# Performance work log

Hardware: AMD Instinct MI355X
Metric: run time of the kernel (lower is better)

Reference implementation:

```python
import jax, jax.numpy as jnp
import numpy as np

EMBED_DIM = 1024
NUM_HEADS = 16
HEAD_DIM = EMBED_DIM // NUM_HEADS
ROPE_BASE = 10000.0


def rotate_half(x):
    # interleaved variant: pairs (x0,x1) -> (-x1, x0)
    x1 = x[..., ::2]
    x2 = x[..., 1::2]
    return jnp.stack((-x2, x1), axis=-1).reshape(x.shape)


def rope_tables(T, dim, dtype):
    inv_freq = 1.0 / (ROPE_BASE ** (jnp.arange(0, dim, 2, dtype=jnp.float32) / dim))
    t = jnp.arange(T, dtype=jnp.float32)
    freqs = t[:, None] * inv_freq[None, :]          # [T, dim/2]
    emb = jnp.concatenate((freqs, freqs), axis=-1)  # [T, dim]
    return jnp.cos(emb).astype(dtype), jnp.sin(emb).astype(dtype)


def setup_inputs() -> dict:
    key = jax.random.key(0)
    kx, kq, ko = jax.random.split(key, 3)
    B, T, D = 2, 2048, EMBED_DIM
    x = jax.random.normal(kx, (B, T, D), dtype=jnp.float32)
    s = 1.0 / np.sqrt(D)
    Wqkv = jax.random.normal(kq, (D, 3 * D), dtype=jnp.float32) * s
    Wout = jax.random.normal(ko, (D, D), dtype=jnp.float32) * s
    return {"x": x, "Wqkv": Wqkv, "Wout": Wout}


def reference(x, Wqkv, Wout):
    B, T, D = x.shape
    H, hd = NUM_HEADS, HEAD_DIM
    qkv = x @ Wqkv                                   # [B,T,3D]
    q, k, v = jnp.split(qkv, 3, axis=-1)
    q = q.reshape(B, T, H, hd).transpose(0, 2, 1, 3)  # [B,H,T,hd]
    k = k.reshape(B, T, H, hd).transpose(0, 2, 1, 3)
    v = v.reshape(B, T, H, hd).transpose(0, 2, 1, 3)
    cos, sin = rope_tables(T, hd, x.dtype)           # [T,hd]
    cos = cos[None, None, :, :]
    sin = sin[None, None, :, :]
    q = q * cos + rotate_half(q) * sin
    k = k * cos + rotate_half(k) * sin
    scale = 1.0 / np.sqrt(hd).astype(np.float32)
    attn = jnp.einsum('bhtd,bhsd->bhts', q, k) * scale  # [B,H,T,T]
    attn = jax.nn.softmax(attn, axis=-1)
    out = jnp.einsum('bhts,bhsd->bhtd', attn, v)     # [B,H,T,hd]
    out = out.transpose(0, 2, 1, 3).reshape(B, T, D)
    return out @ Wout
```

## Files before the change

kernel.cpp:

```cpp
#include <hip/hip_runtime.h>
#include <hip/hip_bf16.h>
#include <stdint.h>


typedef unsigned short u16;
typedef short bf16x8 __attribute__((ext_vector_type(8)));
typedef float f32x4  __attribute__((ext_vector_type(4)));
typedef float f32x16 __attribute__((ext_vector_type(16)));

#if defined(__has_builtin) && __has_builtin(__builtin_amdgcn_exp2f)
#define EXP2F(x) __builtin_amdgcn_exp2f(x)
#else
#define EXP2F(x) exp2f(x)
#endif

__device__ __forceinline__ u16 f2b(float f) {
  uint32_t u = __float_as_uint(f);
  u += 0x7fffu + ((u >> 16) & 1u);
  return (u16)(u >> 16);
}
__device__ __forceinline__ uint32_t pkbf(float a, float b) {
  __hip_bfloat162 h = __float22bfloat162_rn(make_float2(a, b));
  union { __hip_bfloat162 h2; uint32_t u; } cv; cv.h2 = h;
  return cv.u;
}

__device__ __forceinline__ void gl2lds16(const void* g, void* l) {
  __builtin_amdgcn_global_load_lds(
      (const __attribute__((address_space(1))) unsigned int*)g,
      (__attribute__((address_space(3))) unsigned int*)l, 16, 0, 0);
}

__global__ void sniff_kernel(const u16* x, int* flag) {
  __shared__ int cnt;
  if (threadIdx.x == 0) cnt = 0;
  __syncthreads();
  int c = 0;
  for (int i = threadIdx.x; i < 4096; i += 256) {
    float a = fabsf(__uint_as_float(((uint32_t)x[2*i]) << 16));
    if (a > 1e-3f && a < 100.f) c++;
  }
  atomicAdd(&cnt, c);
  __syncthreads();
  if (threadIdx.x == 0) *flag = (cnt > 2048) ? 1 : 0;
}

__device__ __forceinline__ void tr_tile(const void* src, u16* dst, int Kd, int N,
                                        int n0, int k0, int isb, u16* Lt, int tid)
{
  const int r = tid >> 2, cseg = (tid & 3) << 4;
  u16 t[16];
  if (isb) {
    const u16* s = (const u16*)src + (size_t)(k0 + r) * N + n0 + cseg;
    *(uint4*)&t[0] = *(const uint4*)s;
    *(uint4*)&t[8] = *(const uint4*)(s + 8);
  } else {
    const float* s = (const float*)src + (size_t)(k0 + r) * N + n0 + cseg;
    #pragma unroll
    for (int j = 0; j < 4; j++) {
      float4 v = *(const float4*)(s + j * 4);
      t[j*4+0] = f2b(v.x); t[j*4+1] = f2b(v.y); t[j*4+2] = f2b(v.z); t[j*4+3] = f2b(v.w);
    }
  }
  #pragma unroll
  for (int j = 0; j < 16; j++) Lt[(cseg + j) * 72 + r] = t[j];
  __syncthreads();
  const int n = tid >> 2, kseg = (tid & 3) << 4;
  uint4 u0 = *(const uint4*)&Lt[n * 72 + kseg];
  uint4 u1 = *(const uint4*)&Lt[n * 72 + kseg + 8];
  u16* d = dst + (size_t)(n0 + n) * Kd + k0 + kseg;
  *(uint4*)d = u0;
  *(uint4*)(d + 8) = u1;
}

__global__ __launch_bounds__(256) void prep_kernel(
    const void* __restrict__ x, const void* __restrict__ wqkv,
    const void* __restrict__ wout, const int* __restrict__ flag,
    u16* __restrict__ Xb, u16* __restrict__ Wqkvt, u16* __restrict__ Woutt,
    float2* __restrict__ CS)
{
  __shared__ u16 Lt[64 * 72];
  const int isb = *flag;
  const int bid = blockIdx.x, tid = threadIdx.x;
  if (bid < 2048) {
    const size_t i = ((size_t)bid * 256 + tid) * 8;
    if (isb) {
      *(uint4*)&Xb[i] = *(const uint4*)((const u16*)x + i);
    } else {
      const float* s = (const float*)x + i;
      float4 a = *(const float4*)s, b = *(const float4*)(s + 4);
      uint4 p;
      p.x = pkbf(a.x, a.y); p.y = pkbf(a.z, a.w);
      p.z = pkbf(b.x, b.y); p.w = pkbf(b.z, b.w);
      *(uint4*)&Xb[i] = p;
    }
  } else if (bid < 2816) {
    const int b = bid - 2048;
    tr_tile(wqkv, Wqkvt, 1024, 3072, (b % 48) * 64, (b / 48) * 64, isb, Lt, tid);
  } else if (bid < 3072) {
    const int b = bid - 2816;
    tr_tile(wout, Woutt, 1024, 1024, (b % 16) * 64, (b / 16) * 64, isb, Lt, tid);
  } else {
    const int idx = (bid - 3072) * 256 + tid;
    const int t = idx >> 5, f = idx & 31;
    float invf = __expf(-(float)f * 0.2878231366242557f);
    float th = (float)t * invf;
    float sn, cs;
    sincosf(th, &sn, &cs);
    CS[idx] = make_float2(cs, sn);
  }
}

__global__ __launch_bounds__(256) void qkv_kernel(
    const u16* __restrict__ Xb, const u16* __restrict__ Wt,
    const float2* __restrict__ CS,
    u16* __restrict__ Q, u16* __restrict__ K, u16* __restrict__ Vt)
{
  __shared__ u16 As[128 * 64];
  __shared__ u16 Bs[128 * 64];
  const int tid = threadIdx.x;
  const int n0 = blockIdx.x * 128;
  const int m0 = blockIdx.y * 128;
  const int w = tid >> 6, l = tid & 63, lr = l & 15, lq = l >> 4;
  const int mrow0 = (w & 1) * 64;
  const int ncol0 = (w >> 1) * 64;
  const int srow = tid >> 3;
  const int gseg = (tid & 7) ^ (srow & 7);

  const int col0 = n0 + ncol0;
  const int sec = col0 >> 10;
  const int isv = (sec == 2);
  const int h = (col0 >> 6) & 15;

  f32x4 acc[4][4] = {};

  for (int k0 = 0; k0 < 1024; k0 += 64) {
    __syncthreads();
    #pragma unroll
    for (int rd = 0; rd < 4; rd++) {
      const int row = srow + rd * 32;
      gl2lds16(Xb + (size_t)(m0 + row) * 1024 + k0 + gseg * 8, &As[tid * 8 + rd * 2048]);
      gl2lds16(Wt + (size_t)(n0 + row) * 1024 + k0 + gseg * 8, &Bs[tid * 8 + rd * 2048]);
    }
    __syncthreads();
    #pragma unroll
    for (int kc = 0; kc < 2; kc++) {
      bf16x8 af[4], bf[4];
      #pragma unroll
      for (int i = 0; i < 4; i++) {
        const int seg = ((kc << 2) | lq) ^ (lr & 7);
        af[i] = *(const bf16x8*)&As[(mrow0 + i * 16 + lr) * 64 + seg * 8];
        bf[i] = *(const bf16x8*)&Bs[(ncol0 + i * 16 + lr) * 64 + seg * 8];
      }
      if (isv) {
        #pragma unroll
        for (int mb = 0; mb < 4; mb++)
          #pragma unroll
          for (int nb = 0; nb < 4; nb++)
            acc[mb][nb] = __builtin_amdgcn_mfma_f32_16x16x32_bf16(af[mb], bf[nb], acc[mb][nb], 0, 0, 0);
      } else {
        #pragma unroll
        for (int mb = 0; mb < 4; mb++)
          #pragma unroll
          for (int nb = 0; nb < 4; nb++)
            acc[mb][nb] = __builtin_amdgcn_mfma_f32_16x16x32_bf16(bf[nb], af[mb], acc[mb][nb], 0, 0, 0);
      }
    }
  }

  if (isv) {
    #pragma unroll
    for (int mb = 0; mb < 4; mb++) {
      const int row0 = m0 + mrow0 + mb * 16 + lq * 4;
      const int b = row0 >> 11, t0 = row0 & 2047;
      const int tp = (t0 & ~12) | ((t0 & 4) << 1) | ((t0 & 8) >> 1);
      #pragma unroll
      for (int nb = 0; nb < 4; nb++) {
        const int d = nb * 16 + lr;
        uint2 uv;
        uv.x = pkbf(acc[mb][nb][0], acc[mb][nb][1]);
        uv.y = pkbf(acc[mb][nb][2], acc[mb][nb][3]);
        *(uint2*)&Vt[(((size_t)b * 16 + h) * 64 + d) * 2048 + tp] = uv;
      }
    }
  } else {
    u16* dst = (sec == 0) ? Q : K;
    const float qscale = 0.125f * 1.44269504f;
    #pragma unroll
    for (int mb = 0; mb < 4; mb++) {
      const int m = m0 + mrow0 + mb * 16 + lr;
      const int b = m >> 11, t = m & 2047;
      const float* csrow = (const float*)(CS + t * 32);
      #pragma unroll
      for (int nb = 0; nb < 4; nb++) {
        const int d = nb * 16 + lq * 4;
        const int fb = d & 31;
        f32x4 c01 = *(const f32x4*)(csrow + 2 * fb);
        f32x4 c23 = *(const f32x4*)(csrow + 2 * fb + 4);
        float v0 = acc[mb][nb][0], v1 = acc[mb][nb][1];
        float v2 = acc[mb][nb][2], v3 = acc[mb][nb][3];
        float r0 = v0 * c01[0] - v1 * c01[1];
        float r1 = fmaf(v1, c01[2], v0 * c01[3]);
        float r2 = v2 * c23[0] - v3 * c23[1];
        float r3 = fmaf(v3, c23[2], v2 * c23[3]);
        if (sec == 0) { r0 *= qscale; r1 *= qscale; r2 *= qscale; r3 *= qscale; }
        uint2 uv;
        uv.x = pkbf(r0, r1);
        uv.y = pkbf(r2, r3);
        *(uint2*)&dst[(((size_t)b * 16 + h) * 2048 + t) * 64 + d] = uv;
      }
    }
  }
}

__global__ __launch_bounds__(256, 4) void attn_kernel(
    const u16* __restrict__ Q, const u16* __restrict__ K,
    const u16* __restrict__ Vt, u16* __restrict__ ATT,
    float* __restrict__ Op, float* __restrict__ Ls, int ns)
{
  __shared__ u16 Ks[2][64 * 64];
  __shared__ u16 Vs[2][64 * 64];
  const int tid = threadIdx.x;
  const int w = tid >> 6, l = tid & 63;
  const int m5 = l & 31, hi = l >> 5;

  const int nwg = 512 * ns;
  const int bid = blockIdx.x;
  const int swz = (bid & 7) * (nwg >> 3) + (bid >> 3);
  const int per_bh = 16 * ns;
  const int bh = swz / per_bh;
  const int rem = swz - bh * per_bh;
  const int sh = rem & (ns - 1);
  const int qt = rem / ns;

  const int slen = 2048 / ns;
  const int sbeg = sh * slen;
  const size_t base = (size_t)bh * (2048 * 64);
  const int qrow0 = qt * 128 + w * 32;
  const int t_own = qrow0 + m5;

  bf16x8 qf[4];
  #pragma unroll
  for (int kd = 0; kd < 4; kd++)
    qf[kd] = *(const bf16x8*)(Q + base + (size_t)t_own * 64 + kd * 16 + hi * 8);

  f32x16 oa[2] = {};
  float lsum = 0.f;

  const int srow = tid >> 3;

  auto stage = [&](int buf, int s0) {
    #pragma unroll
    for (int rd = 0; rd < 2; rd++) {
      const int row = srow + rd * 32;
      const int gs = (tid & 7) ^ (row & 7) ^ ((row >> 3) & 3);
      gl2lds16(K + base + (size_t)(s0 + row) * 64 + gs * 8, &Ks[buf][tid * 8 + rd * 2048]);
      gl2lds16(Vt + base + (size_t)row * 2048 + s0 + gs * 8, &Vs[buf][tid * 8 + rd * 2048]);
    }
  };

  stage(0, sbeg);
  const int nt = slen >> 6;

  #pragma unroll 1
  for (int t = 0; t < nt; t++) {
    const int buf = t & 1;
    __syncthreads();
    if (t + 1 < nt) stage(buf ^ 1, sbeg + (t + 1) * 64);

    uint32_t pw[2][8];
    #pragma unroll
    for (int sb = 0; sb < 2; sb++) {
      const int row = sb * 32 + m5;
      const int sw = (row & 7) ^ ((row >> 3) & 3);
      bf16x8 kf[4];
      #pragma unroll
      for (int kd = 0; kd < 4; kd++)
        kf[kd] = *(const bf16x8*)&Ks[buf][row * 64 + ((((kd << 1) | hi) ^ sw) << 3)];
      f32x16 z = {};
      __builtin_amdgcn_s_setprio(1);
      z = __builtin_amdgcn_mfma_f32_32x32x16_bf16(kf[0], qf[0], z, 0, 0, 0);
      z = __builtin_amdgcn_mfma_f32_32x32x16_bf16(kf[1], qf[1], z, 0, 0, 0);
      z = __builtin_amdgcn_mfma_f32_32x32x16_bf16(kf[2], qf[2], z, 0, 0, 0);
      z = __builtin_amdgcn_mfma_f32_32x32x16_bf16(kf[3], qf[3], z, 0, 0, 0);
      __builtin_amdgcn_s_setprio(0);
      float e[16];
      #pragma unroll
      for (int r = 0; r < 16; r++) e[r] = EXP2F(z[r]);
      lsum += (((e[0] + e[1]) + (e[2] + e[3])) + ((e[4] + e[5]) + (e[6] + e[7])))
            + (((e[8] + e[9]) + (e[10] + e[11])) + ((e[12] + e[13]) + (e[14] + e[15])));
      #pragma unroll
      for (int w2 = 0; w2 < 8; w2++)
        pw[sb][w2] = pkbf(e[2 * w2], e[2 * w2 + 1]);
    }

    #pragma unroll
    for (int db = 0; db < 2; db++) {
      const int row = db * 32 + m5;
      const int sw = (row & 7) ^ ((row >> 3) & 3);
      bf16x8 vf[4];
      #pragma unroll
      for (int sblk = 0; sblk < 4; sblk++)
        vf[sblk] = *(const bf16x8*)&Vs[buf][row * 64 + ((((sblk << 1) | hi) ^ sw) << 3)];
      __builtin_amdgcn_s_setprio(1);
      #pragma unroll
      for (int sblk = 0; sblk < 4; sblk++) {
        union { uint32_t u[4]; bf16x8 v; } pf;
        const int sb = sblk >> 1, off = (sblk & 1) * 4;
        pf.u[0] = pw[sb][off + 0]; pf.u[1] = pw[sb][off + 1];
        pf.u[2] = pw[sb][off + 2]; pf.u[3] = pw[sb][off + 3];
        oa[db] = __builtin_amdgcn_mfma_f32_32x32x16_bf16(vf[sblk], pf.v, oa[db], 0, 0, 0);
      }
      __builtin_amdgcn_s_setprio(0);
    }
  }

  lsum += __shfl_xor(lsum, 32, 64);

  const int b = bh >> 4, h = bh & 15;
  if (ns == 1) {
    const float inv = 1.f / lsum;
    u16* dst = ATT + ((size_t)(b * 2048 + t_own)) * 1024 + h * 64;
    #pragma unroll
    for (int db = 0; db < 2; db++)
      #pragma unroll
      for (int rq = 0; rq < 4; rq++) {
        const int d0 = db * 32 + rq * 8 + hi * 4;
        uint2 u;
        u.x = pkbf(oa[db][4 * rq + 0] * inv, oa[db][4 * rq + 1] * inv);
        u.y = pkbf(oa[db][4 * rq + 2] * inv, oa[db][4 * rq + 3] * inv);
        *(uint2*)&dst[d0] = u;
      }
  } else {
    float* op = Op + (size_t)sh * (65536ull * 64);
    const size_t row = (size_t)bh * 2048 + t_own;
    #pragma unroll
    for (int db = 0; db < 2; db++)
      #pragma unroll
      for (int rq = 0; rq < 4; rq++) {
        const int d0 = db * 32 + rq * 8 + hi * 4;
        f32x4 v;
        v[0] = oa[db][4 * rq + 0]; v[1] = oa[db][4 * rq + 1];
        v[2] = oa[db][4 * rq + 2]; v[3] = oa[db][4 * rq + 3];
        *(f32x4*)&op[row * 64 + d0] = v;
      }
    if (hi == 0) Ls[(size_t)sh * 65536 + row] = lsum;
  }
}

__global__ __launch_bounds__(256) void combine_kernel(
    const float* __restrict__ Op, const float* __restrict__ Ls, u16* __restrict__ ATT)
{
  const int idx = blockIdx.x * 256 + threadIdx.x;
  const int R = idx >> 3;
  const int c = (idx & 7) * 8;
  const float* p0 = Op + (size_t)R * 64 + c;
  const float* p1 = p0 + 65536ull * 64;
  f32x4 a0 = *(const f32x4*)p0, a1 = *(const f32x4*)(p0 + 4);
  f32x4 b0 = *(const f32x4*)p1, b1 = *(const f32x4*)(p1 + 4);
  const float inv = 1.f / (Ls[R] + Ls[65536 + R]);
  const int bh = R >> 11, trow = R & 2047;
  const int b = bh >> 4, h = bh & 15;
  u16* d = ATT + ((size_t)(b * 2048 + trow)) * 1024 + h * 64 + c;
  uint4 u;
  u.x = pkbf((a0[0] + b0[0]) * inv, (a0[1] + b0[1]) * inv);
  u.y = pkbf((a0[2] + b0[2]) * inv, (a0[3] + b0[3]) * inv);
  u.z = pkbf((a1[0] + b1[0]) * inv, (a1[1] + b1[1]) * inv);
  u.w = pkbf((a1[2] + b1[2]) * inv, (a1[3] + b1[3]) * inv);
  *(uint4*)d = u;
}

__global__ __launch_bounds__(256) void outproj_kernel(
    const u16* __restrict__ A, const u16* __restrict__ Wt,
    const int* __restrict__ flag, void* __restrict__ outv)
{
  __shared__ u16 As[128 * 64];
  __shared__ u16 Bs[128 * 64];
  const int isb = *flag;
  const int tid = threadIdx.x;
  const int n0 = blockIdx.x * 128;
  const int m0 = blockIdx.y * 128;
  const int w = tid >> 6, l = tid & 63, lr = l & 15, lq = l >> 4;
  const int mrow0 = (w & 1) * 64;
  const int ncol0 = (w >> 1) * 64;
  const int srow = tid >> 3;
  const int gseg = (tid & 7) ^ (srow & 7);

  f32x4 acc[4][4] = {};

  for (int k0 = 0; k0 < 1024; k0 += 64) {
    __syncthreads();
    #pragma unroll
    for (int rd = 0; rd < 4; rd++) {
      const int row = srow + rd * 32;
      gl2lds16(A + (size_t)(m0 + row) * 1024 + k0 + gseg * 8, &As[tid * 8 + rd * 2048]);
      gl2lds16(Wt + (size_t)(n0 + row) * 1024 + k0 + gseg * 8, &Bs[tid * 8 + rd * 2048]);
    }
    __syncthreads();
    #pragma unroll
    for (int kc = 0; kc < 2; kc++) {
      bf16x8 af[4], bf[4];
      #pragma unroll
      for (int i = 0; i < 4; i++) {
        const int seg = ((kc << 2) | lq) ^ (lr & 7);
        af[i] = *(const bf16x8*)&As[(mrow0 + i * 16 + lr) * 64 + seg * 8];
        bf[i] = *(const bf16x8*)&Bs[(ncol0 + i * 16 + lr) * 64 + seg * 8];
      }
      #pragma unroll
      for (int mb = 0; mb < 4; mb++)
        #pragma unroll
        for (int nb = 0; nb < 4; nb++)
          acc[mb][nb] = __builtin_amdgcn_mfma_f32_16x16x32_bf16(bf[nb], af[mb], acc[mb][nb], 0, 0, 0);
    }
  }
  #pragma unroll
  for (int mb = 0; mb < 4; mb++) {
    const int row = m0 + mrow0 + mb * 16 + lr;
    #pragma unroll
    for (int nb = 0; nb < 4; nb++) {
      const int col = n0 + ncol0 + nb * 16 + lq * 4;
      f32x4 v = acc[mb][nb];
      if (isb) {
        uint2 uv;
        uv.x = pkbf(v[0], v[1]);
        uv.y = pkbf(v[2], v[3]);
        *(uint2*)&((u16*)outv)[(size_t)row * 1024 + col] = uv;
      } else {
        *(f32x4*)&((float*)outv)[(size_t)row * 1024 + col] = v;
      }
    }
  }
}

extern "C" void kernel_launch(void* const* d_in, const int* in_sizes, int n_in,
                              void* d_out, int out_size, void* d_ws, size_t ws_size,
                              hipStream_t stream)
{
  const void* x    = d_in[0];
  const void* wqkv = d_in[1];
  const void* wout = d_in[2];
  char* ws = (char*)d_ws;
  const size_t MB = 1024 * 1024;
  int*    flag   = (int*)ws;
  float2* CS     = (float2*)(ws + 1024);
  u16*    Xb     = (u16*)(ws + 1 * MB);
  u16*    ATT    = Xb;
  u16*    Wqkvt  = (u16*)(ws + 9 * MB);
  u16*    Woutt  = (u16*)(ws + 15 * MB);
  u16*    Q      = (u16*)(ws + 17 * MB);
  u16*    K      = (u16*)(ws + 25 * MB);
  u16*    Vt     = (u16*)(ws + 33 * MB);
  float*  Op     = (float*)(ws + 41 * MB);
  float*  Ls     = (float*)(ws + 75 * MB);

  const bool split = ws_size >= 76 * MB;
  const int ns = split ? 2 : 1;

  sniff_kernel<<<1, 256, 0, stream>>>((const u16*)x, flag);
  prep_kernel<<<3328, 256, 0, stream>>>(x, wqkv, wout, flag, Xb, Wqkvt, Woutt, CS);
  qkv_kernel<<<dim3(24, 32), 256, 0, stream>>>(Xb, Wqkvt, CS, Q, K, Vt);
  attn_kernel<<<dim3(512 * ns), 256, 0, stream>>>(Q, K, Vt, ATT, Op, Ls, ns);
  if (split)
    combine_kernel<<<2048, 256, 0, stream>>>(Op, Ls, ATT);
  outproj_kernel<<<dim3(8, 32), 256, 0, stream>>>(ATT, Woutt, flag, d_out);
}
```

Measured before the change: 209.5 us.

## Software-pipeline attention loop to overlap QK exp with previous tile's PV

```diff
diff --git a/kernel.cpp b/kernel.cpp
--- a/kernel.cpp
+++ b/kernel.cpp
@@ -246,74 +246,127 @@
 
   f32x16 oa[2] = {};
   float lsum = 0.f;
+  uint32_t pwA[16], pwB[16];
+  bf16x8 vfp[8];
 
   const int srow = tid >> 3;
 
-  auto stage = [&](int buf, int s0) {
+  auto stage = [&](int buf_, int s0) {
     #pragma unroll
     for (int rd = 0; rd < 2; rd++) {
       const int row = srow + rd * 32;
       const int gs = (tid & 7) ^ (row & 7) ^ ((row >> 3) & 3);
-      gl2lds16(K + base + (size_t)(s0 + row) * 64 + gs * 8, &Ks[buf][tid * 8 + rd * 2048]);
-      gl2lds16(Vt + base + (size_t)row * 2048 + s0 + gs * 8, &Vs[buf][tid * 8 + rd * 2048]);
+      gl2lds16(K + base + (size_t)(s0 + row) * 64 + gs * 8, &Ks[buf_][tid * 8 + rd * 2048]);
+      gl2lds16(Vt + base + (size_t)row * 2048 + s0 + gs * 8, &Vs[buf_][tid * 8 + rd * 2048]);
     }
   };
+
+#define KF_S(SB, Z)                                                           \
+  {                                                                           \
+    const int row_ = (SB) * 32 + m5;                                          \
+    const int sw_ = (row_ & 7) ^ ((row_ >> 3) & 3);                           \
+    bf16x8 kf_[4];                                                            \
+    _Pragma("unroll")                                                         \
+    for (int kd = 0; kd < 4; kd++)                                            \
+      kf_[kd] = *(const bf16x8*)&Ks[buf][row_ * 64 + ((((kd << 1) | hi) ^ sw_) << 3)]; \
+    f32x16 zt_ = {};                                                          \
+    __builtin_amdgcn_s_setprio(1);                                            \
+    zt_ = __builtin_amdgcn_mfma_f32_32x32x16_bf16(kf_[0], qf[0], zt_, 0, 0, 0); \
+    zt_ = __builtin_amdgcn_mfma_f32_32x32x16_bf16(kf_[1], qf[1], zt_, 0, 0, 0); \
+    zt_ = __builtin_amdgcn_mfma_f32_32x32x16_bf16(kf_[2], qf[2], zt_, 0, 0, 0); \
+    zt_ = __builtin_amdgcn_mfma_f32_32x32x16_bf16(kf_[3], qf[3], zt_, 0, 0, 0); \
+    __builtin_amdgcn_s_setprio(0);                                            \
+    Z = zt_;                                                                  \
+  }
+
+#define EXPPACK(Z, PW, BASE)                                                  \
+  {                                                                           \
+    float e_[16];                                                             \
+    _Pragma("unroll")                                                         \
+    for (int r = 0; r < 16; r++) e_[r] = EXP2F((Z)[r]);                       \
+    lsum += (((e_[0] + e_[1]) + (e_[2] + e_[3])) + ((e_[4] + e_[5]) + (e_[6] + e_[7]))) \
+          + (((e_[8] + e_[9]) + (e_[10] + e_[11])) + ((e_[12] + e_[13]) + (e_[14] + e_[15]))); \
+    _Pragma("unroll")                                                         \
+    for (int w2 = 0; w2 < 8; w2++) PW[(BASE) + w2] = pkbf(e_[2 * w2], e_[2 * w2 + 1]); \
+  }
+
+#define PVHALF(DB, PW)                                                        \
+  {                                                                           \
+    __builtin_amdgcn_s_setprio(1);                                            \
+    _Pragma("unroll")                                                         \
+    for (int sblk = 0; sblk < 4; sblk++) {                                    \
+      union { uint32_t u[4]; bf16x8 v; } pf_;                                 \
+      const int sb_ = sblk >> 1, off_ = (sblk & 1) * 4;                       \
+      pf_.u[0] = PW[sb_ * 8 + off_ + 0]; pf_.u[1] = PW[sb_ * 8 + off_ + 1];   \
+      pf_.u[2] = PW[sb_ * 8 + off_ + 2]; pf_.u[3] = PW[sb_ * 8 + off_ + 3];   \
+      oa[DB] = __builtin_amdgcn_mfma_f32_32x32x16_bf16(vfp[(DB) * 4 + sblk], pf_.v, oa[DB], 0, 0, 0); \
+    }                                                                         \
+    __builtin_amdgcn_s_setprio(0);                                            \
+  }
+
+#define VFLOAD()                                                              \
+  {                                                                           \
+    _Pragma("unroll")                                                         \
+    for (int db_ = 0; db_ < 2; db_++) {                                       \
+      const int row_ = db_ * 32 + m5;                                         \
+      const int sw_ = (row_ & 7) ^ ((row_ >> 3) & 3);                         \
+      _Pragma("unroll")                                                       \
+      for (int sblk = 0; sblk < 4; sblk++)                                    \
+        vfp[db_ * 4 + sblk] = *(const bf16x8*)&Vs[buf][row_ * 64 + ((((sblk << 1) | hi) ^ sw_) << 3)]; \
+    }                                                                         \
+  }
 
   stage(0, sbeg);
   const int nt = slen >> 6;
+  int buf = 0;
+  f32x16 z;
+
+  __syncthreads();
+  stage(1, sbeg + 64);
+  KF_S(0, z); EXPPACK(z, pwA, 0);
+  KF_S(1, z); EXPPACK(z, pwA, 8);
+  VFLOAD();
+  buf = 1;
 
   #pragma unroll 1
-  for (int t = 0; t < nt; t++) {
-    const int buf = t & 1;
+  for (int t = 1; t + 1 < nt; t += 2) {
     __syncthreads();
-    if (t + 1 < nt) stage(buf ^ 1, sbeg + (t + 1) * 64);
-
-    uint32_t pw[2][8];
-    #pragma unroll
-    for (int sb = 0; sb < 2; sb++) {
-      const int row = sb * 32 + m5;
-      const int sw = (row & 7) ^ ((row >> 3) & 3);
-      bf16x8 kf[4];
-      #pragma unroll
-      for (int kd = 0; kd < 4; kd++)
-        kf[kd] = *(const bf16x8*)&Ks[buf][row * 64 + ((((kd << 1) | hi) ^ sw) << 3)];
-      f32x16 z = {};
-      __builtin_amdgcn_s_setprio(1);
-      z = __builtin_amdgcn_mfma_f32_32x32x16_bf16(kf[0], qf[0], z, 0, 0, 0);
-      z = __builtin_amdgcn_mfma_f32_32x32x16_bf16(kf[1], qf[1], z, 0, 0, 0);
-      z = __builtin_amdgcn_mfma_f32_32x32x16_bf16(kf[2], qf[2], z, 0, 0, 0);
-      z = __builtin_amdgcn_mfma_f32_32x32x16_bf16(kf[3], qf[3], z, 0, 0, 0);
-      __builtin_amdgcn_s_setprio(0);
-      float e[16];
-      #pragma unroll
-      for (int r = 0; r < 16; r++) e[r] = EXP2F(z[r]);
-      lsum += (((e[0] + e[1]) + (e[2] + e[3])) + ((e[4] + e[5]) + (e[6] + e[7])))
-            + (((e[8] + e[9]) + (e[10] + e[11])) + ((e[12] + e[13]) + (e[14] + e[15])));
-      #pragma unroll
-      for (int w2 = 0; w2 < 8; w2++)
-        pw[sb][w2] = pkbf(e[2 * w2], e[2 * w2 + 1]);
-    }
-
-    #pragma unroll
-    for (int db = 0; db < 2; db++) {
-      const int row = db * 32 + m5;
-      const int sw = (row & 7) ^ ((row >> 3) & 3);
-      bf16x8 vf[4];
-      #pragma unroll
-      for (int sblk = 0; sblk < 4; sblk++)
-        vf[sblk] = *(const bf16x8*)&Vs[buf][row * 64 + ((((sblk << 1) | hi) ^ sw) << 3)];
-      __builtin_amdgcn_s_setprio(1);
-      #pragma unroll
-      for (int sblk = 0; sblk < 4; sblk++) {
-        union { uint32_t u[4]; bf16x8 v; } pf;
-        const int sb = sblk >> 1, off = (sblk & 1) * 4;
-        pf.u[0] = pw[sb][off + 0]; pf.u[1] = pw[sb][off + 1];
-        pf.u[2] = pw[sb][off + 2]; pf.u[3] = pw[sb][off + 3];
-        oa[db] = __builtin_amdgcn_mfma_f32_32x32x16_bf16(vf[sblk], pf.v, oa[db], 0, 0, 0);
-      }
-      __builtin_amdgcn_s_setprio(0);
-    }
-  }
+    stage(buf ^ 1, sbeg + (t + 1) * 64);
+    KF_S(0, z);
+    PVHALF(0, pwA);
+    EXPPACK(z, pwB, 0);
+    KF_S(1, z);
+    PVHALF(1, pwA);
+    EXPPACK(z, pwB, 8);
+    VFLOAD();
+    buf ^= 1;
+    __syncthreads();
+    stage(buf ^ 1, sbeg + (t + 2) * 64);
+    KF_S(0, z);
+    PVHALF(0, pwB);
+    EXPPACK(z, pwA, 0);
+    KF_S(1, z);
+    PVHALF(1, pwB);
+    EXPPACK(z, pwA, 8);
+    VFLOAD();
+    buf ^= 1;
+  }
+
+  __syncthreads();
+  KF_S(0, z);
+  PVHALF(0, pwA);
+  EXPPACK(z, pwB, 0);
+  KF_S(1, z);
+  PVHALF(1, pwA);
+  EXPPACK(z, pwB, 8);
+  VFLOAD();
+  PVHALF(0, pwB);
+  PVHALF(1, pwB);
+
+#undef KF_S
+#undef EXPPACK
+#undef PVHALF
+#undef VFLOAD
 
   lsum += __shfl_xor(lsum, 32, 64);
 
```

After: 271.9 us. +29.8%, slower.

## Merge split-KV attention halves within one 512-thread block via LDS

Applied to the files above, without the earlier changes.

```diff
diff --git a/kernel.cpp b/kernel.cpp
--- a/kernel.cpp
+++ b/kernel.cpp
@@ -213,30 +213,26 @@
   }
 }
 
-__global__ __launch_bounds__(256, 4) void attn_kernel(
+__global__ __launch_bounds__(512, 4) void attn_kernel(
     const u16* __restrict__ Q, const u16* __restrict__ K,
-    const u16* __restrict__ Vt, u16* __restrict__ ATT,
-    float* __restrict__ Op, float* __restrict__ Ls, int ns)
-{
-  __shared__ u16 Ks[2][64 * 64];
-  __shared__ u16 Vs[2][64 * 64];
+    const u16* __restrict__ Vt, u16* __restrict__ ATT)
+{
+  __shared__ u16 pool[2][2][2][4096];
   const int tid = threadIdx.x;
-  const int w = tid >> 6, l = tid & 63;
+  const int shard = tid >> 8;
+  const int t2 = tid & 255;
+  const int ws = (tid >> 6) & 3;
+  const int l = tid & 63;
   const int m5 = l & 31, hi = l >> 5;
 
-  const int nwg = 512 * ns;
   const int bid = blockIdx.x;
-  const int swz = (bid & 7) * (nwg >> 3) + (bid >> 3);
-  const int per_bh = 16 * ns;
-  const int bh = swz / per_bh;
-  const int rem = swz - bh * per_bh;
-  const int sh = rem & (ns - 1);
-  const int qt = rem / ns;
-
-  const int slen = 2048 / ns;
-  const int sbeg = sh * slen;
+  const int swz = (bid & 7) * 64 + (bid >> 3);
+  const int bh = swz >> 4;
+  const int qt = swz & 15;
+
+  const int sbeg = shard * 1024;
   const size_t base = (size_t)bh * (2048 * 64);
-  const int qrow0 = qt * 128 + w * 32;
+  const int qrow0 = qt * 128 + ws * 32;
   const int t_own = qrow0 + m5;
 
   bf16x8 qf[4];
@@ -247,26 +243,30 @@
   f32x16 oa[2] = {};
   float lsum = 0.f;
 
-  const int srow = tid >> 3;
+  const int srow = t2 >> 3;
 
   auto stage = [&](int buf, int s0) {
     #pragma unroll
     for (int rd = 0; rd < 2; rd++) {
       const int row = srow + rd * 32;
-      const int gs = (tid & 7) ^ (row & 7) ^ ((row >> 3) & 3);
-      gl2lds16(K + base + (size_t)(s0 + row) * 64 + gs * 8, &Ks[buf][tid * 8 + rd * 2048]);
-      gl2lds16(Vt + base + (size_t)row * 2048 + s0 + gs * 8, &Vs[buf][tid * 8 + rd * 2048]);
+      const int gs = (t2 & 7) ^ (row & 7) ^ ((row >> 3) & 3);
+      gl2lds16(K + base + (size_t)(s0 + row) * 64 + gs * 8,
+               &pool[shard][0][buf][t2 * 8 + rd * 2048]);
+      gl2lds16(Vt + base + (size_t)row * 2048 + s0 + gs * 8,
+               &pool[shard][1][buf][t2 * 8 + rd * 2048]);
     }
   };
 
   stage(0, sbeg);
-  const int nt = slen >> 6;
+  const int nt = 16;
 
   #pragma unroll 1
   for (int t = 0; t < nt; t++) {
     const int buf = t & 1;
     __syncthreads();
     if (t + 1 < nt) stage(buf ^ 1, sbeg + (t + 1) * 64);
+    const u16* Ks = pool[shard][0][buf];
+    const u16* Vs = pool[shard][1][buf];
 
     uint32_t pw[2][8];
     #pragma unroll
@@ -276,7 +276,7 @@
       bf16x8 kf[4];
       #pragma unroll
       for (int kd = 0; kd < 4; kd++)
-        kf[kd] = *(const bf16x8*)&Ks[buf][row * 64 + ((((kd << 1) | hi) ^ sw) << 3)];
+        kf[kd] = *(const bf16x8*)&Ks[row * 64 + ((((kd << 1) | hi) ^ sw) << 3)];
       f32x16 z = {};
       __builtin_amdgcn_s_setprio(1);
       z = __builtin_amdgcn_mfma_f32_32x32x16_bf16(kf[0], qf[0], z, 0, 0, 0);
@@ -301,7 +301,7 @@
       bf16x8 vf[4];
       #pragma unroll
       for (int sblk = 0; sblk < 4; sblk++)
-        vf[sblk] = *(const bf16x8*)&Vs[buf][row * 64 + ((((sblk << 1) | hi) ^ sw) << 3)];
+        vf[sblk] = *(const bf16x8*)&Vs[row * 64 + ((((sblk << 1) | hi) ^ sw) << 3)];
       __builtin_amdgcn_s_setprio(1);
       #pragma unroll
       for (int sblk = 0; sblk < 4; sblk++) {
@@ -317,57 +317,37 @@
 
   lsum += __shfl_xor(lsum, 32, 64);
 
-  const int b = bh >> 4, h = bh & 15;
-  if (ns == 1) {
-    const float inv = 1.f / lsum;
+  float* mo = (float*)pool;
+  __syncthreads();
+  if (shard == 1) {
+    #pragma unroll
+    for (int db = 0; db < 2; db++)
+      #pragma unroll
+      for (int r = 0; r < 16; r++)
+        mo[((ws * 32 + db * 16 + r) << 6) + l] = oa[db][r];
+    mo[8192 + ws * 64 + l] = lsum;
+  }
+  __syncthreads();
+  if (shard == 0) {
+    const float ls2 = mo[8192 + ws * 64 + l];
+    const float inv = 1.f / (lsum + ls2);
+    const int b = bh >> 4, h = bh & 15;
     u16* dst = ATT + ((size_t)(b * 2048 + t_own)) * 1024 + h * 64;
     #pragma unroll
     for (int db = 0; db < 2; db++)
       #pragma unroll
       for (int rq = 0; rq < 4; rq++) {
         const int d0 = db * 32 + rq * 8 + hi * 4;
+        float s0 = oa[db][4 * rq + 0] + mo[((ws * 32 + db * 16 + 4 * rq + 0) << 6) + l];
+        float s1 = oa[db][4 * rq + 1] + mo[((ws * 32 + db * 16 + 4 * rq + 1) << 6) + l];
+        float s2 = oa[db][4 * rq + 2] + mo[((ws * 32 + db * 16 + 4 * rq + 2) << 6) + l];
+        float s3 = oa[db][4 * rq + 3] + mo[((ws * 32 + db * 16 + 4 * rq + 3) << 6) + l];
         uint2 u;
-        u.x = pkbf(oa[db][4 * rq + 0] * inv, oa[db][4 * rq + 1] * inv);
-        u.y = pkbf(oa[db][4 * rq + 2] * inv, oa[db][4 * rq + 3] * inv);
+        u.x = pkbf(s0 * inv, s1 * inv);
+        u.y = pkbf(s2 * inv, s3 * inv);
         *(uint2*)&dst[d0] = u;
       }
-  } else {
-    float* op = Op + (size_t)sh * (65536ull * 64);
-    const size_t row = (size_t)bh * 2048 + t_own;
-    #pragma unroll
-    for (int db = 0; db < 2; db++)
-      #pragma unroll
-      for (int rq = 0; rq < 4; rq++) {
-        const int d0 = db * 32 + rq * 8 + hi * 4;
-        f32x4 v;
-        v[0] = oa[db][4 * rq + 0]; v[1] = oa[db][4 * rq + 1];
-        v[2] = oa[db][4 * rq + 2]; v[3] = oa[db][4 * rq + 3];
-        *(f32x4*)&op[row * 64 + d0] = v;
-      }
-    if (hi == 0) Ls[(size_t)sh * 65536 + row] = lsum;
-  }
-}
-
-__global__ __launch_bounds__(256) void combine_kernel(
-    const float* __restrict__ Op, const float* __restrict__ Ls, u16* __restrict__ ATT)
-{
-  const int idx = blockIdx.x * 256 + threadIdx.x;
-  const int R = idx >> 3;
-  const int c = (idx & 7) * 8;
-  const float* p0 = Op + (size_t)R * 64 + c;
-  const float* p1 = p0 + 65536ull * 64;
-  f32x4 a0 = *(const f32x4*)p0, a1 = *(const f32x4*)(p0 + 4);
-  f32x4 b0 = *(const f32x4*)p1, b1 = *(const f32x4*)(p1 + 4);
-  const float inv = 1.f / (Ls[R] + Ls[65536 + R]);
-  const int bh = R >> 11, trow = R & 2047;
-  const int b = bh >> 4, h = bh & 15;
-  u16* d = ATT + ((size_t)(b * 2048 + trow)) * 1024 + h * 64 + c;
-  uint4 u;
-  u.x = pkbf((a0[0] + b0[0]) * inv, (a0[1] + b0[1]) * inv);
-  u.y = pkbf((a0[2] + b0[2]) * inv, (a0[3] + b0[3]) * inv);
-  u.z = pkbf((a1[0] + b1[0]) * inv, (a1[1] + b1[1]) * inv);
-  u.w = pkbf((a1[2] + b1[2]) * inv, (a1[3] + b1[3]) * inv);
-  *(uint4*)d = u;
+  }
 }
 
 __global__ __launch_bounds__(256) void outproj_kernel(
@@ -450,17 +430,10 @@
   u16*    Q      = (u16*)(ws + 17 * MB);
   u16*    K      = (u16*)(ws + 25 * MB);
   u16*    Vt     = (u16*)(ws + 33 * MB);
-  float*  Op     = (float*)(ws + 41 * MB);
-  float*  Ls     = (float*)(ws + 75 * MB);
-
-  const bool split = ws_size >= 76 * MB;
-  const int ns = split ? 2 : 1;
 
   sniff_kernel<<<1, 256, 0, stream>>>((const u16*)x, flag);
   prep_kernel<<<3328, 256, 0, stream>>>(x, wqkv, wout, flag, Xb, Wqkvt, Woutt, CS);
   qkv_kernel<<<dim3(24, 32), 256, 0, stream>>>(Xb, Wqkvt, CS, Q, K, Vt);
-  attn_kernel<<<dim3(512 * ns), 256, 0, stream>>>(Q, K, Vt, ATT, Op, Ls, ns);
-  if (split)
-    combine_kernel<<<2048, 256, 0, stream>>>(Op, Ls, ATT);
+  attn_kernel<<<dim3(512), 512, 0, stream>>>(Q, K, Vt, ATT);
   outproj_kernel<<<dim3(8, 32), 256, 0, stream>>>(ATT, Woutt, flag, d_out);
 }
```

New measurement: 197.6 us. 5.7% less time.
